# Optimization experiments

Measured on AMD Instinct MI355X. Metric: run time of the kernel, lower is better.

## Reference

```python
import jax, jax.numpy as jnp
import numpy as np

D_FIELDS = 16
HIDDEN = 16
N_POINTS = 1_000_000


def setup_inputs() -> dict:
    key = jax.random.key(0)
    ks = jax.random.split(key, 7)
    x = jax.random.normal(ks[0], (1, 3, N_POINTS), dtype=jnp.float32)
    # stacked per-field Conv1d(k=1) weights: conv weight [out,in,1] -> matrix [out,in]
    W1 = jax.random.normal(ks[1], (D_FIELDS, HIDDEN, 3), dtype=jnp.float32) * 0.1
    b1 = jax.random.normal(ks[2], (D_FIELDS, HIDDEN), dtype=jnp.float32) * 0.1
    W2 = jax.random.normal(ks[3], (D_FIELDS, HIDDEN, HIDDEN), dtype=jnp.float32) * 0.1
    b2 = jax.random.normal(ks[4], (D_FIELDS, HIDDEN), dtype=jnp.float32) * 0.1
    W3 = jax.random.normal(ks[5], (D_FIELDS, 3, HIDDEN), dtype=jnp.float32) * 0.1
    b3 = jax.random.normal(ks[6], (D_FIELDS, 3), dtype=jnp.float32) * 0.1
    return {"x": x, "W1": W1, "b1": b1, "W2": W2, "b2": b2, "W3": W3, "b3": b3, "D": D_FIELDS}


def reference(x, W1, b1, W2, b2, W3, b3, D):
    # x: [1, 3, N]. Original loops d in range(D) applying field d's MLP to x and
    # concatenating along dim 0 -> [D, 3, N]. Fused here as batched GEMMs over d.
    xs = x[0]  # [3, N]
    h = jax.nn.relu(jnp.einsum('dhc,cn->dhn', W1, xs) + b1[:, :, None])      # [D,H,N]
    h = jax.nn.relu(jnp.einsum('dgh,dhn->dgn', W2, h) + b2[:, :, None])      # [D,H,N]
    out = jnp.einsum('doh,dhn->don', W3, h) + b3[:, :, None]                 # [D,3,N]
    return out
```

## Files before the change

### kernel.cpp

```cpp
#include <hip/hip_runtime.h>


#define MFMA16(a, b, c) __builtin_amdgcn_mfma_f32_16x16x16f16((a), (b), (c), 0, 0, 0)

#define GP 5
#define NG 5
#define TILES_PER_WAVE (GP * NG)
#define WAVES_PER_BLOCK 4
#define FPB 2
#define PTS_PER_WAVE (TILES_PER_WAVE * 16)
#define PTS_PER_BLOCK (PTS_PER_WAVE * WAVES_PER_BLOCK)

typedef __fp16 pk16x2 __attribute__((ext_vector_type(2)));
typedef _Float16 half4_t __attribute__((ext_vector_type(4)));
typedef float float4_t __attribute__((ext_vector_type(4)));

union H2I { pk16x2 h; int i; };
union Frag { half4_t v; int i[2]; };

__device__ __forceinline__ int pkrtz(float a, float b) {
    H2I u; u.h = __builtin_amdgcn_cvt_pkrtz(a, b); return u.i;
}

__device__ __forceinline__ int pk_relu_pack(float a, float b) {
    H2I u; u.h = __builtin_amdgcn_cvt_pkrtz(a, b);
    const pk16x2 z = {(__fp16)0.f, (__fp16)0.f};
    u.h = __builtin_elementwise_max(u.h, z);
    return u.i;
}

__global__ __launch_bounds__(256, 4) void fields_r12_kernel(
    const float* __restrict__ x,
    const float* __restrict__ W1, const float* __restrict__ b1,
    const float* __restrict__ W2, const float* __restrict__ b2,
    const float* __restrict__ W3, const float* __restrict__ b3,
    float* __restrict__ out, int N)
{
    const int lane = threadIdx.x & 63;
    const int wave = threadIdx.x >> 6;
    const int q    = lane >> 4;
    const int n16  = lane & 15;

    const int bid = blockIdx.x;
    const int r   = bid & 7;
    const int fg  = (bid >> 3) & 7;
    const int a   = bid >> 6;
    const int chunk  = a * 8 + r;
    const int chunks = (N + PTS_PER_BLOCK - 1) / PTS_PER_BLOCK;
    if (chunk >= chunks) return;

    const int base = chunk * PTS_PER_BLOCK + wave * PTS_PER_WAVE;
    const bool isq0 = (q == 0);

    Frag a1w[FPB], a2w[FPB], a3w[FPB];
    float4_t b1v[FPB], b2v[FPB], b3v[FPB];
#pragma unroll
    for (int f = 0; f < FPB; ++f) {
        const int d = fg * FPB + f;
        const float* w1 = W1 + (d * 16 + n16) * 3;
        a1w[f].v = (half4_t){(_Float16)w1[0], (_Float16)w1[1],
                             (_Float16)w1[2], (_Float16)0.f};
        const float4_t w2 = *(const float4_t*)(W2 + (d * 16 + n16) * 16 + q * 4);
        a2w[f].v = (half4_t){(_Float16)w2.x, (_Float16)w2.y, (_Float16)w2.z,
                             (_Float16)w2.w};
        if (n16 < 3) {
            const float4_t w3 = *(const float4_t*)(W3 + (d * 3 + n16) * 16 + q * 4);
            a3w[f].v = (half4_t){(_Float16)w3.x, (_Float16)w3.y, (_Float16)w3.z,
                                 (_Float16)w3.w};
        } else {
            a3w[f].i[0] = 0; a3w[f].i[1] = 0;
        }
        b1v[f] = *(const float4_t*)(b1 + d * 16 + q * 4);
        b2v[f] = *(const float4_t*)(b2 + d * 16 + q * 4);
        float4_t bb3 = (float4_t){0.f, 0.f, 0.f, 0.f};
        if (isq0) {
            bb3.x = b3[d * 3 + 0];
            bb3.y = b3[d * 3 + 1];
            bb3.z = b3[d * 3 + 2];
        }
        b3v[f] = bb3;
    }

    const float* xb0 = x + base;
    const float* xb1 = xb0 + N;
    const float* xb2 = xb1 + N;
    float* ob[FPB][3];
#pragma unroll
    for (int f = 0; f < FPB; ++f) {
        const int d = fg * FPB + f;
#pragma unroll
        for (int i = 0; i < 3; ++i)
            ob[f][i] = out + (size_t)(d * 3 + i) * N + base;
    }

    if (base + PTS_PER_WAVE <= N) {
        float xb[2][3][GP];
#pragma unroll
        for (int t = 0; t < GP; ++t) {
            xb[0][0][t] = xb0[n16 + t * 16];
            xb[0][1][t] = xb1[n16 + t * 16];
            xb[0][2][t] = xb2[n16 + t * 16];
        }
#pragma unroll
        for (int g = 0; g < NG; ++g) {
            const int b = g & 1;
            if (g + 1 < NG) {
                const int nb = (g + 1) & 1;
#pragma unroll
                for (int t = 0; t < GP; ++t) {
                    const int off = n16 + ((g + 1) * GP + t) * 16;
                    xb[nb][0][t] = xb0[off];
                    xb[nb][1][t] = xb1[off];
                    xb[nb][2][t] = xb2[off];
                }
            }
            Frag xf[GP];
#pragma unroll
            for (int t = 0; t < GP; ++t) {
                const int p01 = pkrtz(xb[b][0][t], xb[b][1][t]);
                const int p2  = pkrtz(xb[b][2][t], 0.f);
                xf[t].i[0] = isq0 ? p01 : 0;
                xf[t].i[1] = isq0 ? p2  : 0;
            }
#pragma unroll
            for (int f = 0; f < FPB; ++f) {
                float4_t acc[GP];
#pragma unroll
                for (int t = 0; t < GP; ++t)
                    acc[t] = MFMA16(a1w[f].v, xf[t].v, b1v[f]);
                Frag hf[GP];
#pragma unroll
                for (int t = 0; t < GP; ++t) {
                    hf[t].i[0] = pk_relu_pack(acc[t].x, acc[t].y);
                    hf[t].i[1] = pk_relu_pack(acc[t].z, acc[t].w);
                }
#pragma unroll
                for (int t = 0; t < GP; ++t)
                    acc[t] = MFMA16(a2w[f].v, hf[t].v, b2v[f]);
#pragma unroll
                for (int t = 0; t < GP; ++t) {
                    hf[t].i[0] = pk_relu_pack(acc[t].x, acc[t].y);
                    hf[t].i[1] = pk_relu_pack(acc[t].z, acc[t].w);
                }
#pragma unroll
                for (int t = 0; t < GP; ++t)
                    acc[t] = MFMA16(a3w[f].v, hf[t].v, b3v[f]);
                if (isq0) {
#pragma unroll
                    for (int t = 0; t < GP; ++t) {
                        const int off = n16 + (g * GP + t) * 16;
                        ob[f][0][off] = acc[t].x;
                        ob[f][1][off] = acc[t].y;
                        ob[f][2][off] = acc[t].z;
                    }
                }
            }
        }
    } else {
#pragma unroll 1
        for (int t = 0; t < TILES_PER_WAVE; ++t) {
            const int off = t * 16;
            const int pt = base + off + n16;
            float x0 = 0.f, x1v = 0.f, x2v = 0.f;
            if (isq0 && pt < N) {
                x0  = xb0[n16 + off];
                x1v = xb1[n16 + off];
                x2v = xb2[n16 + off];
            }
            Frag xf;
            xf.i[0] = pkrtz(x0, x1v);
            xf.i[1] = pkrtz(x2v, 0.f);
#pragma unroll
            for (int f = 0; f < FPB; ++f) {
                float4_t acc = MFMA16(a1w[f].v, xf.v, b1v[f]);
                Frag bf;
                bf.i[0] = pk_relu_pack(acc.x, acc.y);
                bf.i[1] = pk_relu_pack(acc.z, acc.w);
                acc = MFMA16(a2w[f].v, bf.v, b2v[f]);
                Frag cf;
                cf.i[0] = pk_relu_pack(acc.x, acc.y);
                cf.i[1] = pk_relu_pack(acc.z, acc.w);
                acc = MFMA16(a3w[f].v, cf.v, b3v[f]);
                if (isq0 && pt < N) {
                    ob[f][0][n16 + off] = acc.x;
                    ob[f][1][n16 + off] = acc.y;
                    ob[f][2][n16 + off] = acc.z;
                }
            }
        }
    }
}

extern "C" void kernel_launch(void* const* d_in, const int* in_sizes, int n_in,
                              void* d_out, int out_size, void* d_ws, size_t ws_size,
                              hipStream_t stream) {
    const float* x  = (const float*)d_in[0];
    const float* W1 = (const float*)d_in[1];
    const float* b1 = (const float*)d_in[2];
    const float* W2 = (const float*)d_in[3];
    const float* b2 = (const float*)d_in[4];
    const float* W3 = (const float*)d_in[5];
    const float* b3 = (const float*)d_in[6];
    float* out = (float*)d_out;

    const int N = in_sizes[0] / 3;
    const int chunks = (N + PTS_PER_BLOCK - 1) / PTS_PER_BLOCK;
    const int a_max  = (chunks + 7) / 8;
    const int grid   = 8 * 8 * a_max;
    fields_r12_kernel<<<grid, 256, 0, stream>>>(x, W1, b1, W2, b2, W3, b3, out, N);
}
```

Measured before the change: 250.7 us.

## Place layer-3 outputs in per-quad rows so every lane stores output

Builds four shifted copies of the W3 fragment so that the third MFMA for sub-tile s writes its three output rows into quad s's accumulator rows. After four sub-tiles each lane holds one point's outputs, so stores are full 64-lane coalesced writes instead of 16-lane writes. The layout moves from 5x5 tiles per wave to 6 groups of 4 sub-tiles, and boundary handling becomes per-group instead of a whole-wave slow path. The cost is extra registers for the shifted W3 copies, per-lane select instructions, and less MFMA interleaving within a group.

```diff
diff --git a/kernel.cpp b/kernel.cpp
--- a/kernel.cpp
+++ b/kernel.cpp
@@ -3,12 +3,11 @@
 
 #define MFMA16(a, b, c) __builtin_amdgcn_mfma_f32_16x16x16f16((a), (b), (c), 0, 0, 0)
 
-#define GP 5
-#define NG 5
-#define TILES_PER_WAVE (GP * NG)
+#define TPG 4
+#define NG 6
 #define WAVES_PER_BLOCK 4
 #define FPB 2
-#define PTS_PER_WAVE (TILES_PER_WAVE * 16)
+#define PTS_PER_WAVE (NG * TPG * 16)
 #define PTS_PER_BLOCK (PTS_PER_WAVE * WAVES_PER_BLOCK)
 
 typedef __fp16 pk16x2 __attribute__((ext_vector_type(2)));
@@ -29,7 +28,7 @@
     return u.i;
 }
 
-__global__ __launch_bounds__(256, 4) void fields_r12_kernel(
+__global__ __launch_bounds__(256, 4) void fields_r13_kernel(
     const float* __restrict__ x,
     const float* __restrict__ W1, const float* __restrict__ b1,
     const float* __restrict__ W2, const float* __restrict__ b2,
@@ -51,8 +50,11 @@
 
     const int base = chunk * PTS_PER_BLOCK + wave * PTS_PER_WAVE;
     const bool isq0 = (q == 0);
-
-    Frag a1w[FPB], a2w[FPB], a3w[FPB];
+    const bool isq1 = (q == 1);
+    const bool isq2 = (q == 2);
+    const bool isq3 = (q == 3);
+
+    Frag a1w[FPB], a2w[FPB], a3w[FPB][TPG];
     float4_t b1v[FPB], b2v[FPB], b3v[FPB];
 #pragma unroll
     for (int f = 0; f < FPB; ++f) {
@@ -63,27 +65,25 @@
         const float4_t w2 = *(const float4_t*)(W2 + (d * 16 + n16) * 16 + q * 4);
         a2w[f].v = (half4_t){(_Float16)w2.x, (_Float16)w2.y, (_Float16)w2.z,
                              (_Float16)w2.w};
-        if (n16 < 3) {
-            const float4_t w3 = *(const float4_t*)(W3 + (d * 3 + n16) * 16 + q * 4);
-            a3w[f].v = (half4_t){(_Float16)w3.x, (_Float16)w3.y, (_Float16)w3.z,
-                                 (_Float16)w3.w};
-        } else {
-            a3w[f].i[0] = 0; a3w[f].i[1] = 0;
+#pragma unroll
+        for (int s = 0; s < TPG; ++s) {
+            const int m = n16 - 4 * s;
+            if (m >= 0 && m < 3) {
+                const float4_t w3 = *(const float4_t*)(W3 + (d * 3 + m) * 16 + q * 4);
+                a3w[f][s].v = (half4_t){(_Float16)w3.x, (_Float16)w3.y,
+                                        (_Float16)w3.z, (_Float16)w3.w};
+            } else {
+                a3w[f][s].i[0] = 0; a3w[f][s].i[1] = 0;
+            }
         }
         b1v[f] = *(const float4_t*)(b1 + d * 16 + q * 4);
         b2v[f] = *(const float4_t*)(b2 + d * 16 + q * 4);
-        float4_t bb3 = (float4_t){0.f, 0.f, 0.f, 0.f};
-        if (isq0) {
-            bb3.x = b3[d * 3 + 0];
-            bb3.y = b3[d * 3 + 1];
-            bb3.z = b3[d * 3 + 2];
-        }
-        b3v[f] = bb3;
-    }
-
-    const float* xb0 = x + base;
-    const float* xb1 = xb0 + N;
-    const float* xb2 = xb1 + N;
+        b3v[f] = (float4_t){b3[d * 3 + 0], b3[d * 3 + 1], b3[d * 3 + 2], 0.f};
+    }
+
+    const float* xp0 = x + base;
+    const float* xp1 = xp0 + N;
+    const float* xp2 = xp1 + N;
     float* ob[FPB][3];
 #pragma unroll
     for (int f = 0; f < FPB; ++f) {
@@ -93,98 +93,93 @@
             ob[f][i] = out + (size_t)(d * 3 + i) * N + base;
     }
 
-    if (base + PTS_PER_WAVE <= N) {
-        float xb[2][3][GP];
-#pragma unroll
-        for (int t = 0; t < GP; ++t) {
-            xb[0][0][t] = xb0[n16 + t * 16];
-            xb[0][1][t] = xb1[n16 + t * 16];
-            xb[0][2][t] = xb2[n16 + t * 16];
+    float xb[2][3][TPG];
+    if (base + 64 <= N) {
+#pragma unroll
+        for (int s = 0; s < TPG; ++s) {
+            xb[0][0][s] = xp0[n16 + s * 16];
+            xb[0][1][s] = xp1[n16 + s * 16];
+            xb[0][2][s] = xp2[n16 + s * 16];
         }
-#pragma unroll
-        for (int g = 0; g < NG; ++g) {
-            const int b = g & 1;
-            if (g + 1 < NG) {
+    }
+
+#pragma unroll
+    for (int g = 0; g < NG; ++g) {
+        const int b = g & 1;
+        if (base + (g + 1) * 64 <= N) {
+            if (g + 1 < NG && base + (g + 2) * 64 <= N) {
                 const int nb = (g + 1) & 1;
 #pragma unroll
-                for (int t = 0; t < GP; ++t) {
-                    const int off = n16 + ((g + 1) * GP + t) * 16;
-                    xb[nb][0][t] = xb0[off];
-                    xb[nb][1][t] = xb1[off];
-                    xb[nb][2][t] = xb2[off];
-                }
-            }
-            Frag xf[GP];
-#pragma unroll
-            for (int t = 0; t < GP; ++t) {
-                const int p01 = pkrtz(xb[b][0][t], xb[b][1][t]);
-                const int p2  = pkrtz(xb[b][2][t], 0.f);
-                xf[t].i[0] = isq0 ? p01 : 0;
-                xf[t].i[1] = isq0 ? p2  : 0;
+                for (int s = 0; s < TPG; ++s) {
+                    const int off = n16 + ((g + 1) * TPG + s) * 16;
+                    xb[nb][0][s] = xp0[off];
+                    xb[nb][1][s] = xp1[off];
+                    xb[nb][2][s] = xp2[off];
+                }
+            }
+            Frag xf[TPG];
+#pragma unroll
+            for (int s = 0; s < TPG; ++s) {
+                const int p01 = pkrtz(xb[b][0][s], xb[b][1][s]);
+                const int p2  = pkrtz(xb[b][2][s], 0.f);
+                xf[s].i[0] = isq0 ? p01 : 0;
+                xf[s].i[1] = isq0 ? p2  : 0;
             }
 #pragma unroll
             for (int f = 0; f < FPB; ++f) {
-                float4_t acc[GP];
-#pragma unroll
-                for (int t = 0; t < GP; ++t)
-                    acc[t] = MFMA16(a1w[f].v, xf[t].v, b1v[f]);
-                Frag hf[GP];
-#pragma unroll
-                for (int t = 0; t < GP; ++t) {
-                    hf[t].i[0] = pk_relu_pack(acc[t].x, acc[t].y);
-                    hf[t].i[1] = pk_relu_pack(acc[t].z, acc[t].w);
-                }
-#pragma unroll
-                for (int t = 0; t < GP; ++t)
-                    acc[t] = MFMA16(a2w[f].v, hf[t].v, b2v[f]);
-#pragma unroll
-                for (int t = 0; t < GP; ++t) {
-                    hf[t].i[0] = pk_relu_pack(acc[t].x, acc[t].y);
-                    hf[t].i[1] = pk_relu_pack(acc[t].z, acc[t].w);
-                }
-#pragma unroll
-                for (int t = 0; t < GP; ++t)
-                    acc[t] = MFMA16(a3w[f].v, hf[t].v, b3v[f]);
-                if (isq0) {
-#pragma unroll
-                    for (int t = 0; t < GP; ++t) {
-                        const int off = n16 + (g * GP + t) * 16;
-                        ob[f][0][off] = acc[t].x;
-                        ob[f][1][off] = acc[t].y;
-                        ob[f][2][off] = acc[t].z;
+                float mo0 = 0.f, mo1 = 0.f, mo2 = 0.f;
+#pragma unroll
+                for (int s = 0; s < TPG; ++s) {
+                    float4_t acc = MFMA16(a1w[f].v, xf[s].v, b1v[f]);
+                    Frag hf;
+                    hf.i[0] = pk_relu_pack(acc.x, acc.y);
+                    hf.i[1] = pk_relu_pack(acc.z, acc.w);
+                    acc = MFMA16(a2w[f].v, hf.v, b2v[f]);
+                    hf.i[0] = pk_relu_pack(acc.x, acc.y);
+                    hf.i[1] = pk_relu_pack(acc.z, acc.w);
+                    acc = MFMA16(a3w[f][s].v, hf.v, b3v[f]);
+                    if (s == 0) { mo0 = acc.x; mo1 = acc.y; mo2 = acc.z; }
+                    else {
+                        const bool sel = (s == 1) ? isq1 : (s == 2) ? isq2 : isq3;
+                        mo0 = sel ? acc.x : mo0;
+                        mo1 = sel ? acc.y : mo1;
+                        mo2 = sel ? acc.z : mo2;
                     }
                 }
-            }
-        }
-    } else {
-#pragma unroll 1
-        for (int t = 0; t < TILES_PER_WAVE; ++t) {
-            const int off = t * 16;
-            const int pt = base + off + n16;
-            float x0 = 0.f, x1v = 0.f, x2v = 0.f;
-            if (isq0 && pt < N) {
-                x0  = xb0[n16 + off];
-                x1v = xb1[n16 + off];
-                x2v = xb2[n16 + off];
-            }
-            Frag xf;
-            xf.i[0] = pkrtz(x0, x1v);
-            xf.i[1] = pkrtz(x2v, 0.f);
-#pragma unroll
-            for (int f = 0; f < FPB; ++f) {
-                float4_t acc = MFMA16(a1w[f].v, xf.v, b1v[f]);
-                Frag bf;
-                bf.i[0] = pk_relu_pack(acc.x, acc.y);
-                bf.i[1] = pk_relu_pack(acc.z, acc.w);
-                acc = MFMA16(a2w[f].v, bf.v, b2v[f]);
-                Frag cf;
-                cf.i[0] = pk_relu_pack(acc.x, acc.y);
-                cf.i[1] = pk_relu_pack(acc.z, acc.w);
-                acc = MFMA16(a3w[f].v, cf.v, b3v[f]);
+                const int off = lane + g * 64;
+                ob[f][0][off] = mo0;
+                ob[f][1][off] = mo1;
+                ob[f][2][off] = mo2;
+            }
+        } else if (base + g * 64 < N) {
+#pragma unroll
+            for (int s = 0; s < TPG; ++s) {
+                const int off = (g * TPG + s) * 16;
+                const int pt = base + off + n16;
+                float x0 = 0.f, x1v = 0.f, x2v = 0.f;
                 if (isq0 && pt < N) {
-                    ob[f][0][n16 + off] = acc.x;
-                    ob[f][1][n16 + off] = acc.y;
-                    ob[f][2][n16 + off] = acc.z;
+                    x0  = xp0[n16 + off];
+                    x1v = xp1[n16 + off];
+                    x2v = xp2[n16 + off];
+                }
+                Frag xf1;
+                xf1.i[0] = pkrtz(x0, x1v);
+                xf1.i[1] = pkrtz(x2v, 0.f);
+#pragma unroll
+                for (int f = 0; f < FPB; ++f) {
+                    float4_t acc = MFMA16(a1w[f].v, xf1.v, b1v[f]);
+                    Frag hf;
+                    hf.i[0] = pk_relu_pack(acc.x, acc.y);
+                    hf.i[1] = pk_relu_pack(acc.z, acc.w);
+                    acc = MFMA16(a2w[f].v, hf.v, b2v[f]);
+                    hf.i[0] = pk_relu_pack(acc.x, acc.y);
+                    hf.i[1] = pk_relu_pack(acc.z, acc.w);
+                    acc = MFMA16(a3w[f][0].v, hf.v, b3v[f]);
+                    if (isq0 && pt < N) {
+                        ob[f][0][n16 + off] = acc.x;
+                        ob[f][1][n16 + off] = acc.y;
+                        ob[f][2][n16 + off] = acc.z;
+                    }
                 }
             }
         }
@@ -207,5 +202,5 @@
     const int chunks = (N + PTS_PER_BLOCK - 1) / PTS_PER_BLOCK;
     const int a_max  = (chunks + 7) / 8;
     const int grid   = 8 * 8 * a_max;
-    fields_r12_kernel<<<grid, 256, 0, stream>>>(x, W1, b1, W2, b2, W3, b3, out, N);
-}
+    fields_r13_kernel<<<grid, 256, 0, stream>>>(x, W1, b1, W2, b2, W3, b3, out, N);
+}
```

New measurement: 252.3 us. Within noise of the previous version (+0.7%).
